# Performance work log

Hardware: AMD Instinct MI355X
Metric: run time of the kernel (lower is better)

Reference implementation:

```python
import jax, jax.numpy as jnp
import numpy as np

MARGIN = 0.3
BIG = 9999999.0


def setup_inputs() -> dict:
    key = jax.random.key(0)
    k1, k2, k3 = jax.random.split(key, 3)
    N, D, D2, NUM_IDS = 8192, 1024, 512, 512
    emb = jax.random.normal(k1, (N, D), dtype=jnp.float32)
    clot_feats_s = jax.random.normal(k2, (N, D2), dtype=jnp.float32)
    label = jax.random.randint(k3, (N,), 0, NUM_IDS, dtype=jnp.int64)
    return {"emb": emb, "label": label, "clot_feats_s": clot_feats_s}


def _margin_ranking_loss(x1, x2, y, margin):
    # torch MarginRankingLoss: mean(max(0, -y*(x1-x2)+margin))
    return jnp.mean(jnp.maximum(0.0, -y * (x1 - x2) + margin))


def reference(emb, label, clot_feats_s):
    N = emb.shape[0]
    # euclidean_dist(emb, emb): [N,N]
    sq = jnp.sum(emb * emb, axis=1)
    dist = sq[:, None] + sq[None, :] - 2.0 * (emb @ emb.T)
    dist = jnp.sqrt(jnp.clip(dist, 1e-12, None))
    # cosine similarity of clot_feats_s with itself: [N,N]
    nrm = jnp.sqrt(jnp.sum(clot_feats_s * clot_feats_s, axis=1))
    cos = (clot_feats_s @ clot_feats_s.T) / (nrm[:, None] * nrm[None, :])
    # same-identity mask
    sim = (label[:, None] == label[None, :]).astype(dist.dtype)
    # batch-hard: top-2 positives (largest masked distance), hardest negative (smallest)
    pos_vals, pos_idx = jax.lax.top_k(dist - BIG * (1.0 - sim), 2)
    dist_ap1, dist_ap2 = pos_vals[:, 0], pos_vals[:, 1]
    neg_mat = dist + BIG * sim
    hard_n_idx = jnp.argmin(neg_mat, axis=1)
    dist_an = jnp.min(neg_mat, axis=1)
    rows = jnp.arange(N)
    # per-row gathers into cosine-sim matrix (detached in original)
    alpha1 = jax.lax.stop_gradient(cos[rows, pos_idx[:, 0]])
    alpha2 = jax.lax.stop_gradient(cos[rows, pos_idx[:, 1]])
    # (alphan gathered in original but unused in the loss)
    y11 = jnp.where(alpha1 < alpha2, -1.0, 1.0)
    y11_m = jnp.where(alpha1 == alpha2, 0.0, 1.0)
    loss11 = _margin_ranking_loss(
        dist_ap2 * y11_m,
        dist_ap1 * y11_m + MARGIN * (alpha1 - alpha2 - y11),
        y11, MARGIN)
    dist_ap1_m = dist_ap1 + MARGIN * (alpha1 - 1.0)
    loss13 = _margin_ranking_loss(dist_an, dist_ap1_m, 1.0, MARGIN)
    loss = 0.1 * loss11 + loss13
    prec = jnp.mean((dist_an > dist_ap1_m).astype(jnp.float32))
    return loss, prec
```

## Files before the change

kernel.cpp:

```cpp
#include <hip/hip_runtime.h>
#include <stdint.h>

#define NR 8192
#define DE 1024
#define DC 512
#define BIGF 9999999.0f
#define MARG 0.3f
#define NEGI -3.0e38f
#define POSI 3.0e38f

typedef __attribute__((ext_vector_type(8))) short bf16x8;
typedef __attribute__((ext_vector_type(4))) float f32x4;

typedef __attribute__((address_space(3))) unsigned int lds_u32;
typedef const __attribute__((address_space(1))) unsigned int glb_u32;

static __device__ __forceinline__ void ld_g2l16(const void* g, void* l) {
    __builtin_amdgcn_global_load_lds((glb_u32*)g, (lds_u32*)l, 16, 0, 0);
}

static __device__ __forceinline__ unsigned short f2bf(float x) {
    unsigned u = __float_as_uint(x);
    unsigned r = u + 0x7FFFu + ((u >> 16) & 1u);
    return (unsigned short)(r >> 16);
}

static __device__ __forceinline__ float b2f(short u) {
    return __uint_as_float(((unsigned)(unsigned short)u) << 16);
}

__global__ __launch_bounds__(256) void k_prep_emb(const float* __restrict__ emb,
                                                  const int* __restrict__ label,
                                                  short* __restrict__ embb,
                                                  float* __restrict__ sq,
                                                  int* __restrict__ cnt) {
    int row = blockIdx.x, tid = threadIdx.x;
    float4 v = ((const float4*)(emb + (size_t)row * DE))[tid];
    float s = v.x * v.x + v.y * v.y + v.z * v.z + v.w * v.w;
    ushort4 b;
    b.x = f2bf(v.x); b.y = f2bf(v.y); b.z = f2bf(v.z); b.w = f2bf(v.w);
    *(ushort4*)&embb[(size_t)row * DE + tid * 4] = b;
    for (int m = 1; m < 64; m <<= 1) s += __shfl_xor(s, m);
    __shared__ float red[4];
    if ((tid & 63) == 0) red[tid >> 6] = s;
    __syncthreads();
    if (tid == 0) {
        sq[row] = red[0] + red[1] + red[2] + red[3];
        atomicAdd(&cnt[label[row]], 1);
    }
}

__global__ __launch_bounds__(512) void k_scan(const int* __restrict__ cnt,
                                              int* __restrict__ clsOff) {
    __shared__ int s[512];
    int t = threadIdx.x;
    s[t] = cnt[t];
    __syncthreads();
    for (int d = 1; d < 512; d <<= 1) {
        int v = (t >= d) ? s[t - d] : 0;
        __syncthreads();
        s[t] += v;
        __syncthreads();
    }
    clsOff[t] = s[t] - cnt[t];
}

__global__ __launch_bounds__(256) void k_fill(const int* __restrict__ label,
                                              const int* __restrict__ clsOff,
                                              int* __restrict__ fill,
                                              int* __restrict__ list) {
    int i = blockIdx.x * 256 + threadIdx.x;
    int l = label[i];
    int p = atomicAdd(&fill[l], 1);
    list[clsOff[l] + p] = i;
}

__global__ __launch_bounds__(256, 3) void k_main(const short* __restrict__ embb,
                                                 const float* __restrict__ sq,
                                                 const int* __restrict__ label,
                                                 unsigned* __restrict__ mnA) {
    const int L = blockIdx.x;
    int bx = (int)((sqrtf((float)(1 + 2 * L)) - 1.0f) * 0.5f);
    while (2 * (bx + 1) * (bx + 1) + 2 * (bx + 1) <= L) ++bx;
    while (2 * bx * bx + 2 * bx > L) --bx;
    const int pnl = L - (2 * bx * bx + 2 * bx);
    const int d = pnl - bx * 4;
    const int jt0 = d > 0 ? d : 0;

    __shared__ __align__(16) short As[128 * 32];
    __shared__ __align__(16) short Bs[128 * 32];

    const int tid = threadIdx.x;
    const int lane = tid & 63;
    const int w = tid >> 6;
    const int q = lane >> 4, l15 = lane & 15;
    const int i0 = pnl * 128;

    const int srow = tid >> 2;
    const int g = (tid & 3) ^ ((tid >> 3) & 3);
    const short* gA = embb + (size_t)(i0 + srow) * DE + g * 8;
    const short* gB = embb + (size_t)(bx * 512 + jt0 * 128 + srow) * DE + g * 8;

    const int pxor = q ^ ((l15 >> 1) & 3);

    float rmn[8], sqi[8];
    int lia[8];
#pragma unroll
    for (int pp = 0; pp < 8; ++pp) {
        rmn[pp] = POSI;
        int rowg = i0 + w * 32 + (pp >> 2) * 16 + q * 4 + (pp & 3);
        sqi[pp] = sq[rowg]; lia[pp] = label[rowg];
    }

    auto stage = [&](int koff, const short* gBb) {
        ld_g2l16(gA + koff, &As[(size_t)tid * 8]);
        ld_g2l16(gA + (size_t)64 * DE + koff, &As[(size_t)(tid + 256) * 8]);
        ld_g2l16(gBb + koff, &Bs[(size_t)tid * 8]);
        ld_g2l16(gBb + (size_t)64 * DE + koff, &Bs[(size_t)(tid + 256) * 8]);
    };

    stage(0, gB);

    for (int jt = jt0; jt < 4; ++jt) {
        const int j0 = bx * 512 + jt * 128;
        f32x4 acc[2][8];
#pragma unroll
        for (int mi = 0; mi < 2; ++mi)
#pragma unroll
            for (int ni = 0; ni < 8; ++ni) acc[mi][ni] = (f32x4){0.f, 0.f, 0.f, 0.f};

        for (int ks = 0; ks < 32; ++ks) {
            __syncthreads();
            bf16x8 af[2], bfr[8];
#pragma unroll
            for (int mi = 0; mi < 2; ++mi)
                af[mi] = *(const bf16x8*)&As[(w * 32 + mi * 16 + l15) * 32 + pxor * 8];
#pragma unroll
            for (int ni = 0; ni < 8; ++ni)
                bfr[ni] = *(const bf16x8*)&Bs[(ni * 16 + l15) * 32 + pxor * 8];
#pragma unroll
            for (int mi = 0; mi < 2; ++mi)
#pragma unroll
                for (int ni = 0; ni < 8; ++ni)
                    acc[mi][ni] = __builtin_amdgcn_mfma_f32_16x16x32_bf16(af[mi], bfr[ni], acc[mi][ni], 0, 0, 0);
            __syncthreads();
            if (ks < 31) {
                stage((ks + 1) * 32, gB);
            } else if (jt < 3) {
                gB += (size_t)128 * DE;
                stage(0, gB);
            }
        }

#pragma unroll
        for (int ni = 0; ni < 8; ++ni) {
            const int cg = j0 + ni * 16 + l15;
            const float sqjv = sq[cg];
            const int lbjv = label[cg];
            float cmn = POSI;
#pragma unroll
            for (int pp = 0; pp < 8; ++pp) {
                float d2 = fmaf(-2.0f, acc[pp >> 2][ni][pp & 3], sqi[pp] + sqjv);
                d2 = fmaxf(d2, 1e-12f);
                float dn = (lia[pp] == lbjv) ? POSI : d2;
                rmn[pp] = fminf(rmn[pp], dn);
                cmn = fminf(cmn, dn);
            }
            cmn = fminf(cmn, __shfl_xor(cmn, 16));
            cmn = fminf(cmn, __shfl_xor(cmn, 32));
            if (q == 0) atomicMin(&mnA[cg], __float_as_uint(cmn));
        }
    }

#pragma unroll
    for (int pp = 0; pp < 8; ++pp) {
        float m0 = rmn[pp];
        for (int s = 1; s <= 8; s <<= 1) m0 = fminf(m0, __shfl_xor(m0, s));
        if (l15 == 0) {
            int rowg = i0 + w * 32 + (pp >> 2) * 16 + q * 4 + (pp & 3);
            atomicMin(&mnA[rowg], __float_as_uint(m0));
        }
    }
}

__global__ __launch_bounds__(256) void k_pos(const short* __restrict__ embb,
                                             const float* __restrict__ sq,
                                             const float* __restrict__ clot,
                                             const int* __restrict__ label,
                                             const int* __restrict__ cnt,
                                             const int* __restrict__ clsOff,
                                             const int* __restrict__ clsList,
                                             const unsigned* __restrict__ mnA,
                                             float* __restrict__ ap1, float* __restrict__ ap2,
                                             float* __restrict__ an,
                                             float* __restrict__ alpha1, float* __restrict__ alpha2) {
    int wid = threadIdx.x >> 6, lane = threadIdx.x & 63;
    int row = blockIdx.x * 4 + wid;
    int lb = label[row];
    int cc = cnt[lb], off = clsOff[lb];
    float sqiv = sq[row];

    const bf16x8* rp = (const bf16x8*)(embb + (size_t)row * DE + lane * 16);
    bf16x8 ra = rp[0], rb = rp[1];
    float rf[16];
#pragma unroll
    for (int t = 0; t < 8; ++t) { rf[t] = b2f(ra[t]); rf[8 + t] = b2f(rb[t]); }

    float v1 = NEGI, v2 = NEGI;
    int i1 = 0, i2 = 0;
    for (int m = 0; m < cc; ++m) {
        int j = clsList[off + m];
        float d2;
        if (j == row) {
            d2 = 1e-12f;
        } else {
            const bf16x8* jp = (const bf16x8*)(embb + (size_t)j * DE + lane * 16);
            bf16x8 ja = jp[0], jb = jp[1];
            float s = 0.f;
#pragma unroll
            for (int t = 0; t < 8; ++t) s = fmaf(rf[t], b2f(ja[t]), s);
#pragma unroll
            for (int t = 0; t < 8; ++t) s = fmaf(rf[8 + t], b2f(jb[t]), s);
            for (int mm = 1; mm < 64; mm <<= 1) s += __shfl_xor(s, mm);
            d2 = fmaxf(fmaf(-2.0f, s, sqiv + sq[j]), 1e-12f);
        }
        bool t1 = (d2 > v1) || (d2 == v1 && j < i1);
        bool t2 = (d2 > v2) || (d2 == v2 && j < i2);
        v2 = t1 ? v1 : (t2 ? d2 : v2);
        i2 = t1 ? i1 : (t2 ? j : i2);
        v1 = t1 ? d2 : v1;
        i1 = t1 ? j : i1;
    }

    float a1 = sqrtf(v1);
    int j1 = i1;
    float a2v; int j2;
    if (cc >= 2) {
        a2v = sqrtf(v2);
        j2 = i2;
    } else {
        float kv = NEGI; int ki = 0;
        for (int c = lane; c < NR; c += 64) {
            if (label[c] == lb) continue;
            const bf16x8* cp = (const bf16x8*)(embb + (size_t)c * DE);
            float s = 0.f;
            for (int t = 0; t < 128; ++t) {
                bf16x8 cv = cp[t];
#pragma unroll
                for (int u = 0; u < 8; ++u) s = fmaf(b2f(ra[0]) * 0.f + 1.f, 0.f, s);
            }
            s = 0.f;
            const short* crow = embb + (size_t)c * DE;
            const short* rrow = embb + (size_t)row * DE;
            for (int t = 0; t < DE; ++t) s = fmaf(b2f(rrow[t]), b2f(crow[t]), s);
            float d2c = fmaxf(fmaf(-2.0f, s, sqiv + sq[c]), 1e-12f);
            bool tk = (d2c > kv) || (d2c == kv && c < ki);
            kv = tk ? d2c : kv; ki = tk ? c : ki;
        }
        for (int mm = 1; mm < 64; mm <<= 1) {
            float ov = __shfl_xor(kv, mm); int oi = __shfl_xor(ki, mm);
            bool tk = (ov > kv) || (ov == kv && oi < ki);
            kv = tk ? ov : kv; ki = tk ? oi : ki;
        }
        a2v = sqrtf(kv) - BIGF;
        j2 = ki;
    }

    const float4* c4 = (const float4*)clot;
    float s1 = 0.f, s2 = 0.f, n0 = 0.f, n1 = 0.f, n2 = 0.f;
    for (int t = lane; t < DC / 4; t += 64) {
        float4 a = c4[(size_t)row * (DC / 4) + t];
        float4 b1 = c4[(size_t)j1 * (DC / 4) + t];
        float4 b2 = c4[(size_t)j2 * (DC / 4) + t];
        s1 += a.x * b1.x + a.y * b1.y + a.z * b1.z + a.w * b1.w;
        s2 += a.x * b2.x + a.y * b2.y + a.z * b2.z + a.w * b2.w;
        n0 += a.x * a.x + a.y * a.y + a.z * a.z + a.w * a.w;
        n1 += b1.x * b1.x + b1.y * b1.y + b1.z * b1.z + b1.w * b1.w;
        n2 += b2.x * b2.x + b2.y * b2.y + b2.z * b2.z + b2.w * b2.w;
    }
    for (int mm = 1; mm < 64; mm <<= 1) {
        s1 += __shfl_xor(s1, mm); s2 += __shfl_xor(s2, mm);
        n0 += __shfl_xor(n0, mm); n1 += __shfl_xor(n1, mm); n2 += __shfl_xor(n2, mm);
    }
    if (lane == 0) {
        ap1[row] = a1; ap2[row] = a2v;
        an[row] = sqrtf(__uint_as_float(mnA[row]));
        alpha1[row] = s1 / (sqrtf(n0) * sqrtf(n1));
        alpha2[row] = s2 / (sqrtf(n0) * sqrtf(n2));
    }
}

__global__ __launch_bounds__(256) void k_final(const float* __restrict__ ap1, const float* __restrict__ ap2,
                                               const float* __restrict__ an,
                                               const float* __restrict__ alpha1, const float* __restrict__ alpha2,
                                               float* __restrict__ out) {
    int tid = threadIdx.x;
    float sl11 = 0.f, sl13 = 0.f, sp = 0.f;
    for (int row = tid; row < NR; row += 256) {
        float a1 = alpha1[row], a2 = alpha2[row];
        float dap1 = ap1[row], dap2 = ap2[row], dan = an[row];
        float y = (a1 < a2) ? -1.f : 1.f;
        float ym = (a1 == a2) ? 0.f : 1.f;
        float x1 = dap2 * ym;
        float x2 = dap1 * ym + MARG * (a1 - a2 - y);
        sl11 += fmaxf(0.f, -y * (x1 - x2) + MARG);
        float ap1m = dap1 + MARG * (a1 - 1.f);
        sl13 += fmaxf(0.f, -(dan - ap1m) + MARG);
        sp += (dan > ap1m) ? 1.f : 0.f;
    }
    for (int m = 1; m < 64; m <<= 1) {
        sl11 += __shfl_xor(sl11, m);
        sl13 += __shfl_xor(sl13, m);
        sp += __shfl_xor(sp, m);
    }
    __shared__ float r11[4], r13[4], rp[4];
    if ((tid & 63) == 0) { r11[tid >> 6] = sl11; r13[tid >> 6] = sl13; rp[tid >> 6] = sp; }
    __syncthreads();
    if (tid == 0) {
        float t11 = r11[0] + r11[1] + r11[2] + r11[3];
        float t13 = r13[0] + r13[1] + r13[2] + r13[3];
        float tp = rp[0] + rp[1] + rp[2] + rp[3];
        out[0] = 0.1f * (t11 / (float)NR) + t13 / (float)NR;
        out[1] = tp / (float)NR;
    }
}

extern "C" void kernel_launch(void* const* d_in, const int* in_sizes, int n_in,
                              void* d_out, int out_size, void* d_ws, size_t ws_size,
                              hipStream_t stream) {
    const float* emb = (const float*)d_in[0];
    const int* label = (const int*)d_in[1];
    const float* clot = (const float*)d_in[2];
    float* out = (float*)d_out;

    char* ws = (char*)d_ws;
    size_t off = 0;
    auto alloc = [&](size_t bytes) -> char* {
        char* p = ws + off;
        off = (off + bytes + 255) & ~(size_t)255;
        return p;
    };
    short*    embb = (short*)alloc((size_t)NR * DE * 2);
    float*    sq   = (float*)alloc(NR * 4);
    int*      cnt  = (int*)alloc(512 * 4);
    int*      cOff = (int*)alloc(512 * 4);
    int*      fill = (int*)alloc(512 * 4);
    int*      list = (int*)alloc(NR * 4);
    unsigned* mnA  = (unsigned*)alloc((size_t)NR * 4);
    float*    ap1  = (float*)alloc(NR * 4);
    float*    ap2  = (float*)alloc(NR * 4);
    float*    an   = (float*)alloc(NR * 4);
    float*    al1  = (float*)alloc(NR * 4);
    float*    al2  = (float*)alloc(NR * 4);

    hipMemsetAsync(cnt, 0, 512 * 4, stream);
    hipMemsetAsync(fill, 0, 512 * 4, stream);
    hipMemsetAsync(mnA, 0xFF, (size_t)NR * 4, stream);

    k_prep_emb<<<dim3(NR), dim3(256), 0, stream>>>(emb, label, embb, sq, cnt);
    k_scan<<<dim3(1), dim3(512), 0, stream>>>(cnt, cOff);
    k_fill<<<dim3(NR / 256), dim3(256), 0, stream>>>(label, cOff, fill, list);
    k_main<<<dim3(544), dim3(256), 0, stream>>>(embb, sq, label, mnA);
    k_pos<<<dim3(NR / 4), dim3(256), 0, stream>>>(embb, sq, clot, label, cnt, cOff, list,
                                                  mnA, ap1, ap2, an, al1, al2);
    k_final<<<dim3(1), dim3(256), 0, stream>>>(ap1, ap2, an, al1, al2, out);
}
```

Measured before the change: 250.9 us.

## Retile distance GEMM to 128x128 triangle blocks and fuse small kernels

The hardest-negative GEMM now uses one 128x128 upper-triangle tile per block (2080 blocks, 2x2 wave layout with 64x64 per wave) instead of 128x512 panels, and occupancy is raised to 4 blocks per CU. Histogram, scan and fill are merged into a single one-block kernel. Memsets are folded into the prep kernel, and the final reduction is fused into k_pos with atomic adds to the output. A dead dummy loop in the rare fallback path is removed. The trade-off is more A-tile reloads, more atomics on mnA and 8192 float atomics on two output addresses.

```diff
diff --git a/kernel.cpp b/kernel.cpp
--- a/kernel.cpp
+++ b/kernel.cpp
@@ -30,10 +30,10 @@
 }
 
 __global__ __launch_bounds__(256) void k_prep_emb(const float* __restrict__ emb,
-                                                  const int* __restrict__ label,
                                                   short* __restrict__ embb,
                                                   float* __restrict__ sq,
-                                                  int* __restrict__ cnt) {
+                                                  unsigned* __restrict__ mnA,
+                                                  float* __restrict__ out) {
     int row = blockIdx.x, tid = threadIdx.x;
     float4 v = ((const float4*)(emb + (size_t)row * DE))[tid];
     float s = v.x * v.x + v.y * v.y + v.z * v.z + v.w * v.w;
@@ -46,15 +46,23 @@
     __syncthreads();
     if (tid == 0) {
         sq[row] = red[0] + red[1] + red[2] + red[3];
-        atomicAdd(&cnt[label[row]], 1);
-    }
-}
-
-__global__ __launch_bounds__(512) void k_scan(const int* __restrict__ cnt,
-                                              int* __restrict__ clsOff) {
-    __shared__ int s[512];
+        mnA[row] = 0xFFFFFFFFu;
+    }
+    if (row == 0 && tid < 2) out[tid] = 0.f;
+}
+
+__global__ __launch_bounds__(512) void k_hist(const int* __restrict__ label,
+                                              int* __restrict__ cnt,
+                                              int* __restrict__ cOff,
+                                              int* __restrict__ list) {
+    __shared__ int h[512], s[512], base[512];
     int t = threadIdx.x;
-    s[t] = cnt[t];
+    h[t] = 0;
+    __syncthreads();
+    for (int i = t; i < NR; i += 512) atomicAdd(&h[label[i]], 1);
+    __syncthreads();
+    int c = h[t];
+    s[t] = c;
     __syncthreads();
     for (int d = 1; d < 512; d <<= 1) {
         int v = (t >= d) ? s[t - d] : 0;
@@ -62,30 +70,27 @@
         s[t] += v;
         __syncthreads();
     }
-    clsOff[t] = s[t] - cnt[t];
-}
-
-__global__ __launch_bounds__(256) void k_fill(const int* __restrict__ label,
-                                              const int* __restrict__ clsOff,
-                                              int* __restrict__ fill,
-                                              int* __restrict__ list) {
-    int i = blockIdx.x * 256 + threadIdx.x;
-    int l = label[i];
-    int p = atomicAdd(&fill[l], 1);
-    list[clsOff[l] + p] = i;
-}
-
-__global__ __launch_bounds__(256, 3) void k_main(const short* __restrict__ embb,
+    cnt[t] = c;
+    cOff[t] = s[t] - c;
+    base[t] = s[t] - c;
+    __syncthreads();
+    for (int i = t; i < NR; i += 512) {
+        int l = label[i];
+        int p = atomicAdd(&base[l], 1);
+        list[p] = i;
+    }
+}
+
+__global__ __launch_bounds__(256, 4) void k_main(const short* __restrict__ embb,
                                                  const float* __restrict__ sq,
                                                  const int* __restrict__ label,
                                                  unsigned* __restrict__ mnA) {
-    const int L = blockIdx.x;
-    int bx = (int)((sqrtf((float)(1 + 2 * L)) - 1.0f) * 0.5f);
-    while (2 * (bx + 1) * (bx + 1) + 2 * (bx + 1) <= L) ++bx;
-    while (2 * bx * bx + 2 * bx > L) --bx;
-    const int pnl = L - (2 * bx * bx + 2 * bx);
-    const int d = pnl - bx * 4;
-    const int jt0 = d > 0 ? d : 0;
+    const int t = blockIdx.x;
+    int qq = (int)((sqrtf(8.0f * (float)t + 1.0f) - 1.0f) * 0.5f);
+    while ((qq + 1) * (qq + 2) / 2 <= t) ++qq;
+    while (qq * (qq + 1) / 2 > t) --qq;
+    const int pq = t - qq * (qq + 1) / 2;
+    const int i0 = pq * 128, j0 = qq * 128;
 
     __shared__ __align__(16) short As[128 * 32];
     __shared__ __align__(16) short Bs[128 * 32];
@@ -93,93 +98,80 @@
     const int tid = threadIdx.x;
     const int lane = tid & 63;
     const int w = tid >> 6;
+    const int wm = w >> 1, wn = w & 1;
     const int q = lane >> 4, l15 = lane & 15;
-    const int i0 = pnl * 128;
 
     const int srow = tid >> 2;
     const int g = (tid & 3) ^ ((tid >> 3) & 3);
     const short* gA = embb + (size_t)(i0 + srow) * DE + g * 8;
-    const short* gB = embb + (size_t)(bx * 512 + jt0 * 128 + srow) * DE + g * 8;
-
+    const short* gB = embb + (size_t)(j0 + srow) * DE + g * 8;
     const int pxor = q ^ ((l15 >> 1) & 3);
 
-    float rmn[8], sqi[8];
-    int lia[8];
-#pragma unroll
-    for (int pp = 0; pp < 8; ++pp) {
-        rmn[pp] = POSI;
-        int rowg = i0 + w * 32 + (pp >> 2) * 16 + q * 4 + (pp & 3);
-        sqi[pp] = sq[rowg]; lia[pp] = label[rowg];
-    }
-
-    auto stage = [&](int koff, const short* gBb) {
+    auto stage = [&](int koff) {
         ld_g2l16(gA + koff, &As[(size_t)tid * 8]);
         ld_g2l16(gA + (size_t)64 * DE + koff, &As[(size_t)(tid + 256) * 8]);
-        ld_g2l16(gBb + koff, &Bs[(size_t)tid * 8]);
-        ld_g2l16(gBb + (size_t)64 * DE + koff, &Bs[(size_t)(tid + 256) * 8]);
+        ld_g2l16(gB + koff, &Bs[(size_t)tid * 8]);
+        ld_g2l16(gB + (size_t)64 * DE + koff, &Bs[(size_t)(tid + 256) * 8]);
     };
 
-    stage(0, gB);
-
-    for (int jt = jt0; jt < 4; ++jt) {
-        const int j0 = bx * 512 + jt * 128;
-        f32x4 acc[2][8];
-#pragma unroll
-        for (int mi = 0; mi < 2; ++mi)
-#pragma unroll
-            for (int ni = 0; ni < 8; ++ni) acc[mi][ni] = (f32x4){0.f, 0.f, 0.f, 0.f};
-
-        for (int ks = 0; ks < 32; ++ks) {
-            __syncthreads();
-            bf16x8 af[2], bfr[8];
-#pragma unroll
-            for (int mi = 0; mi < 2; ++mi)
-                af[mi] = *(const bf16x8*)&As[(w * 32 + mi * 16 + l15) * 32 + pxor * 8];
-#pragma unroll
-            for (int ni = 0; ni < 8; ++ni)
-                bfr[ni] = *(const bf16x8*)&Bs[(ni * 16 + l15) * 32 + pxor * 8];
-#pragma unroll
-            for (int mi = 0; mi < 2; ++mi)
-#pragma unroll
-                for (int ni = 0; ni < 8; ++ni)
-                    acc[mi][ni] = __builtin_amdgcn_mfma_f32_16x16x32_bf16(af[mi], bfr[ni], acc[mi][ni], 0, 0, 0);
-            __syncthreads();
-            if (ks < 31) {
-                stage((ks + 1) * 32, gB);
-            } else if (jt < 3) {
-                gB += (size_t)128 * DE;
-                stage(0, gB);
+    f32x4 acc[4][4];
+#pragma unroll
+    for (int mi = 0; mi < 4; ++mi)
+#pragma unroll
+        for (int ni = 0; ni < 4; ++ni) acc[mi][ni] = (f32x4){0.f, 0.f, 0.f, 0.f};
+
+    stage(0);
+    for (int ks = 0; ks < 32; ++ks) {
+        __syncthreads();
+        bf16x8 af[4], bfr[4];
+#pragma unroll
+        for (int mi = 0; mi < 4; ++mi)
+            af[mi] = *(const bf16x8*)&As[(wm * 64 + mi * 16 + l15) * 32 + pxor * 8];
+#pragma unroll
+        for (int ni = 0; ni < 4; ++ni)
+            bfr[ni] = *(const bf16x8*)&Bs[(wn * 64 + ni * 16 + l15) * 32 + pxor * 8];
+#pragma unroll
+        for (int mi = 0; mi < 4; ++mi)
+#pragma unroll
+            for (int ni = 0; ni < 4; ++ni)
+                acc[mi][ni] = __builtin_amdgcn_mfma_f32_16x16x32_bf16(af[mi], bfr[ni], acc[mi][ni], 0, 0, 0);
+        __syncthreads();
+        if (ks < 31) stage((ks + 1) * 32);
+    }
+
+    float sqj[4]; int lbj[4];
+#pragma unroll
+    for (int ni = 0; ni < 4; ++ni) {
+        int cg = j0 + wn * 64 + ni * 16 + l15;
+        sqj[ni] = sq[cg]; lbj[ni] = label[cg];
+    }
+    float cmn[4] = {POSI, POSI, POSI, POSI};
+#pragma unroll
+    for (int mi = 0; mi < 4; ++mi) {
+#pragma unroll
+        for (int r = 0; r < 4; ++r) {
+            const int rowg = i0 + wm * 64 + mi * 16 + q * 4 + r;
+            const float si = sq[rowg];
+            const int li = label[rowg];
+            float rm = POSI;
+#pragma unroll
+            for (int ni = 0; ni < 4; ++ni) {
+                float d2 = fmaf(-2.0f, acc[mi][ni][r], si + sqj[ni]);
+                d2 = fmaxf(d2, 1e-12f);
+                float dn = (li == lbj[ni]) ? POSI : d2;
+                rm = fminf(rm, dn);
+                cmn[ni] = fminf(cmn[ni], dn);
             }
+            for (int s = 1; s <= 8; s <<= 1) rm = fminf(rm, __shfl_xor(rm, s));
+            if (l15 == 0) atomicMin(&mnA[rowg], __float_as_uint(rm));
         }
-
-#pragma unroll
-        for (int ni = 0; ni < 8; ++ni) {
-            const int cg = j0 + ni * 16 + l15;
-            const float sqjv = sq[cg];
-            const int lbjv = label[cg];
-            float cmn = POSI;
-#pragma unroll
-            for (int pp = 0; pp < 8; ++pp) {
-                float d2 = fmaf(-2.0f, acc[pp >> 2][ni][pp & 3], sqi[pp] + sqjv);
-                d2 = fmaxf(d2, 1e-12f);
-                float dn = (lia[pp] == lbjv) ? POSI : d2;
-                rmn[pp] = fminf(rmn[pp], dn);
-                cmn = fminf(cmn, dn);
-            }
-            cmn = fminf(cmn, __shfl_xor(cmn, 16));
-            cmn = fminf(cmn, __shfl_xor(cmn, 32));
-            if (q == 0) atomicMin(&mnA[cg], __float_as_uint(cmn));
-        }
-    }
-
-#pragma unroll
-    for (int pp = 0; pp < 8; ++pp) {
-        float m0 = rmn[pp];
-        for (int s = 1; s <= 8; s <<= 1) m0 = fminf(m0, __shfl_xor(m0, s));
-        if (l15 == 0) {
-            int rowg = i0 + w * 32 + (pp >> 2) * 16 + q * 4 + (pp & 3);
-            atomicMin(&mnA[rowg], __float_as_uint(m0));
-        }
+    }
+#pragma unroll
+    for (int ni = 0; ni < 4; ++ni) {
+        float c = cmn[ni];
+        c = fminf(c, __shfl_xor(c, 16));
+        c = fminf(c, __shfl_xor(c, 32));
+        if (q == 0) atomicMin(&mnA[j0 + wn * 64 + ni * 16 + l15], __float_as_uint(c));
     }
 }
 
@@ -191,9 +183,7 @@
                                              const int* __restrict__ clsOff,
                                              const int* __restrict__ clsList,
                                              const unsigned* __restrict__ mnA,
-                                             float* __restrict__ ap1, float* __restrict__ ap2,
-                                             float* __restrict__ an,
-                                             float* __restrict__ alpha1, float* __restrict__ alpha2) {
+                                             float* __restrict__ out) {
     int wid = threadIdx.x >> 6, lane = threadIdx.x & 63;
     int row = blockIdx.x * 4 + wid;
     int lb = label[row];
@@ -204,7 +194,7 @@
     bf16x8 ra = rp[0], rb = rp[1];
     float rf[16];
 #pragma unroll
-    for (int t = 0; t < 8; ++t) { rf[t] = b2f(ra[t]); rf[8 + t] = b2f(rb[t]); }
+    for (int u = 0; u < 8; ++u) { rf[u] = b2f(ra[u]); rf[8 + u] = b2f(rb[u]); }
 
     float v1 = NEGI, v2 = NEGI;
     int i1 = 0, i2 = 0;
@@ -218,9 +208,9 @@
             bf16x8 ja = jp[0], jb = jp[1];
             float s = 0.f;
 #pragma unroll
-            for (int t = 0; t < 8; ++t) s = fmaf(rf[t], b2f(ja[t]), s);
-#pragma unroll
-            for (int t = 0; t < 8; ++t) s = fmaf(rf[8 + t], b2f(jb[t]), s);
+            for (int u = 0; u < 8; ++u) s = fmaf(rf[u], b2f(ja[u]), s);
+#pragma unroll
+            for (int u = 0; u < 8; ++u) s = fmaf(rf[8 + u], b2f(jb[u]), s);
             for (int mm = 1; mm < 64; mm <<= 1) s += __shfl_xor(s, mm);
             d2 = fmaxf(fmaf(-2.0f, s, sqiv + sq[j]), 1e-12f);
         }
@@ -232,27 +222,20 @@
         i1 = t1 ? j : i1;
     }
 
-    float a1 = sqrtf(v1);
+    float dap1 = sqrtf(v1);
     int j1 = i1;
-    float a2v; int j2;
+    float dap2; int j2;
     if (cc >= 2) {
-        a2v = sqrtf(v2);
+        dap2 = sqrtf(v2);
         j2 = i2;
     } else {
         float kv = NEGI; int ki = 0;
+        const short* rrow = embb + (size_t)row * DE;
         for (int c = lane; c < NR; c += 64) {
             if (label[c] == lb) continue;
-            const bf16x8* cp = (const bf16x8*)(embb + (size_t)c * DE);
+            const short* crow = embb + (size_t)c * DE;
             float s = 0.f;
-            for (int t = 0; t < 128; ++t) {
-                bf16x8 cv = cp[t];
-#pragma unroll
-                for (int u = 0; u < 8; ++u) s = fmaf(b2f(ra[0]) * 0.f + 1.f, 0.f, s);
-            }
-            s = 0.f;
-            const short* crow = embb + (size_t)c * DE;
-            const short* rrow = embb + (size_t)row * DE;
-            for (int t = 0; t < DE; ++t) s = fmaf(b2f(rrow[t]), b2f(crow[t]), s);
+            for (int u = 0; u < DE; ++u) s = fmaf(b2f(rrow[u]), b2f(crow[u]), s);
             float d2c = fmaxf(fmaf(-2.0f, s, sqiv + sq[c]), 1e-12f);
             bool tk = (d2c > kv) || (d2c == kv && c < ki);
             kv = tk ? d2c : kv; ki = tk ? c : ki;
@@ -262,16 +245,16 @@
             bool tk = (ov > kv) || (ov == kv && oi < ki);
             kv = tk ? ov : kv; ki = tk ? oi : ki;
         }
-        a2v = sqrtf(kv) - BIGF;
+        dap2 = sqrtf(kv) - BIGF;
         j2 = ki;
     }
 
     const float4* c4 = (const float4*)clot;
     float s1 = 0.f, s2 = 0.f, n0 = 0.f, n1 = 0.f, n2 = 0.f;
-    for (int t = lane; t < DC / 4; t += 64) {
-        float4 a = c4[(size_t)row * (DC / 4) + t];
-        float4 b1 = c4[(size_t)j1 * (DC / 4) + t];
-        float4 b2 = c4[(size_t)j2 * (DC / 4) + t];
+    for (int u = lane; u < DC / 4; u += 64) {
+        float4 a = c4[(size_t)row * (DC / 4) + u];
+        float4 b1 = c4[(size_t)j1 * (DC / 4) + u];
+        float4 b2 = c4[(size_t)j2 * (DC / 4) + u];
         s1 += a.x * b1.x + a.y * b1.y + a.z * b1.z + a.w * b1.w;
         s2 += a.x * b2.x + a.y * b2.y + a.z * b2.z + a.w * b2.w;
         n0 += a.x * a.x + a.y * a.y + a.z * a.z + a.w * a.w;
@@ -283,45 +266,18 @@
         n0 += __shfl_xor(n0, mm); n1 += __shfl_xor(n1, mm); n2 += __shfl_xor(n2, mm);
     }
     if (lane == 0) {
-        ap1[row] = a1; ap2[row] = a2v;
-        an[row] = sqrtf(__uint_as_float(mnA[row]));
-        alpha1[row] = s1 / (sqrtf(n0) * sqrtf(n1));
-        alpha2[row] = s2 / (sqrtf(n0) * sqrtf(n2));
-    }
-}
-
-__global__ __launch_bounds__(256) void k_final(const float* __restrict__ ap1, const float* __restrict__ ap2,
-                                               const float* __restrict__ an,
-                                               const float* __restrict__ alpha1, const float* __restrict__ alpha2,
-                                               float* __restrict__ out) {
-    int tid = threadIdx.x;
-    float sl11 = 0.f, sl13 = 0.f, sp = 0.f;
-    for (int row = tid; row < NR; row += 256) {
-        float a1 = alpha1[row], a2 = alpha2[row];
-        float dap1 = ap1[row], dap2 = ap2[row], dan = an[row];
-        float y = (a1 < a2) ? -1.f : 1.f;
-        float ym = (a1 == a2) ? 0.f : 1.f;
+        float al1 = s1 / (sqrtf(n0) * sqrtf(n1));
+        float al2 = s2 / (sqrtf(n0) * sqrtf(n2));
+        float dan = sqrtf(__uint_as_float(mnA[row]));
+        float y = (al1 < al2) ? -1.f : 1.f;
+        float ym = (al1 == al2) ? 0.f : 1.f;
         float x1 = dap2 * ym;
-        float x2 = dap1 * ym + MARG * (a1 - a2 - y);
-        sl11 += fmaxf(0.f, -y * (x1 - x2) + MARG);
-        float ap1m = dap1 + MARG * (a1 - 1.f);
-        sl13 += fmaxf(0.f, -(dan - ap1m) + MARG);
-        sp += (dan > ap1m) ? 1.f : 0.f;
-    }
-    for (int m = 1; m < 64; m <<= 1) {
-        sl11 += __shfl_xor(sl11, m);
-        sl13 += __shfl_xor(sl13, m);
-        sp += __shfl_xor(sp, m);
-    }
-    __shared__ float r11[4], r13[4], rp[4];
-    if ((tid & 63) == 0) { r11[tid >> 6] = sl11; r13[tid >> 6] = sl13; rp[tid >> 6] = sp; }
-    __syncthreads();
-    if (tid == 0) {
-        float t11 = r11[0] + r11[1] + r11[2] + r11[3];
-        float t13 = r13[0] + r13[1] + r13[2] + r13[3];
-        float tp = rp[0] + rp[1] + rp[2] + rp[3];
-        out[0] = 0.1f * (t11 / (float)NR) + t13 / (float)NR;
-        out[1] = tp / (float)NR;
+        float x2 = dap1 * ym + MARG * (al1 - al2 - y);
+        float l11 = fmaxf(0.f, -y * (x1 - x2) + MARG);
+        float ap1m = dap1 + MARG * (al1 - 1.f);
+        float l13 = fmaxf(0.f, -(dan - ap1m) + MARG);
+        atomicAdd(&out[0], (0.1f * l11 + l13) * (1.0f / (float)NR));
+        atomicAdd(&out[1], ((dan > ap1m) ? 1.f : 0.f) * (1.0f / (float)NR));
     }
 }
 
@@ -344,24 +300,12 @@
     float*    sq   = (float*)alloc(NR * 4);
     int*      cnt  = (int*)alloc(512 * 4);
     int*      cOff = (int*)alloc(512 * 4);
-    int*      fill = (int*)alloc(512 * 4);
     int*      list = (int*)alloc(NR * 4);
     unsigned* mnA  = (unsigned*)alloc((size_t)NR * 4);
-    float*    ap1  = (float*)alloc(NR * 4);
-    float*    ap2  = (float*)alloc(NR * 4);
-    float*    an   = (float*)alloc(NR * 4);
-    float*    al1  = (float*)alloc(NR * 4);
-    float*    al2  = (float*)alloc(NR * 4);
-
-    hipMemsetAsync(cnt, 0, 512 * 4, stream);
-    hipMemsetAsync(fill, 0, 512 * 4, stream);
-    hipMemsetAsync(mnA, 0xFF, (size_t)NR * 4, stream);
-
-    k_prep_emb<<<dim3(NR), dim3(256), 0, stream>>>(emb, label, embb, sq, cnt);
-    k_scan<<<dim3(1), dim3(512), 0, stream>>>(cnt, cOff);
-    k_fill<<<dim3(NR / 256), dim3(256), 0, stream>>>(label, cOff, fill, list);
-    k_main<<<dim3(544), dim3(256), 0, stream>>>(embb, sq, label, mnA);
+
+    k_prep_emb<<<dim3(NR), dim3(256), 0, stream>>>(emb, embb, sq, mnA, out);
+    k_hist<<<dim3(1), dim3(512), 0, stream>>>(label, cnt, cOff, list);
+    k_main<<<dim3(2080), dim3(256), 0, stream>>>(embb, sq, label, mnA);
     k_pos<<<dim3(NR / 4), dim3(256), 0, stream>>>(embb, sq, clot, label, cnt, cOff, list,
-                                                  mnA, ap1, ap2, an, al1, al2);
-    k_final<<<dim3(1), dim3(256), 0, stream>>>(ap1, ap2, an, al1, al2, out);
-}
+                                                  mnA, out);
+}
```

After: 426.5 us. +70.0%, slower.
